# Performance work log

Hardware: AMD Instinct MI355X
Metric: run time of the kernel (lower is better)

## Reference

```python
import jax, jax.numpy as jnp
import numpy as np
import math

B, C, RES, N, H = 32, 32, 16, 16384, 64
G = RES ** 3
RATIO = 1.0


def _halton2(n):
    # 2-D Halton sequence (radical inverse, bases 2 and 3), shape (2, n)
    def radinv(idx, base):
        inv = np.zeros(n, dtype=np.float64)
        f = 1.0 / base
        i = idx.copy()
        while i.max() > 0:
            inv += f * (i % base)
            i //= base
            f /= base
        return inv
    idx = np.arange(1, n + 1)
    return np.stack([radinv(idx, 2), radinv(idx, 3)], axis=0).astype(np.float32)


def setup_inputs() -> dict:
    key = jax.random.key(0)
    ks = jax.random.split(key, 3)
    rng = np.random.default_rng(0)
    x = jax.random.normal(ks[0], (B, C, RES, RES, RES), dtype=jnp.float32)
    # density-driven counts: per-batch multinomial allocation summing exactly to N
    dens = rng.random((B, G)) ** 2
    probs = dens / dens.sum(axis=1, keepdims=True)
    counts = np.stack([rng.multinomial(N, probs[b]) for b in range(B)]).astype(np.int32)
    # grid offsets: ((meshgrid + 0.5) / res - 0.5).view(3, -1)  (normalize_ratio = 0.5)
    grid = np.stack(np.meshgrid(np.arange(RES), np.arange(RES), np.arange(RES), indexing='ij'), 0).astype(np.float32)
    grid_o = ((grid + 0.5) / RES - 0.5).reshape(3, -1)
    # Halton noise scaled: b_rnd * ratio - ratio/2, broadcast to batch
    b_rnd = _halton2(N) * RATIO - RATIO / 2.0
    b_rnd = np.broadcast_to(b_rnd[None], (B, 2, N)).copy()
    # pointwise generator MLP: (C+2) -> H -> 3
    W1 = jax.random.normal(ks[1], (H, C + 2), dtype=jnp.float32) * 0.05
    b1 = jnp.zeros((H,), dtype=jnp.float32)
    W2 = jax.random.normal(ks[2], (3, H), dtype=jnp.float32) * 0.05
    b2 = jnp.zeros((3,), dtype=jnp.float32)
    return {"x": x, "counts": jnp.asarray(counts), "b_rnd": jnp.asarray(b_rnd),
            "grid_o": jnp.asarray(grid_o), "W1": W1, "b1": b1, "W2": W2, "b2": b2}


def reference(x, counts, b_rnd, grid_o, W1, b1, W2, b2):
    b, c = x.shape[0], x.shape[1]
    n = b_rnd.shape[-1]
    xf = x.reshape(b, c, -1)                      # (b, c, G)
    # repeat_interleave(x[:, ind], counts[ind]) with fixed output size n:
    # output slot j maps to cell idx = searchsorted(cumsum(counts), j, 'right')
    cum = jnp.cumsum(counts, axis=1)              # (b, G)
    slots = jnp.arange(n)
    idx = jax.vmap(lambda cs: jnp.searchsorted(cs, slots, side='right'))(cum)  # (b, n)
    x_ind = jnp.take_along_axis(xf, idx[:, None, :], axis=2)                   # (b, c, n)
    o_ind = jnp.transpose(grid_o[:, idx], (1, 0, 2))                           # (b, 3, n)
    b_inp = jnp.concatenate([x_ind, b_rnd], axis=1)                            # (b, c+2, n)
    h = jax.nn.relu(jnp.einsum('hc,bcn->bhn', W1, b_inp) + b1[None, :, None])
    out = jnp.einsum('oh,bhn->bon', W2, h) + b2[None, :, None]                 # (b, 3, n)
    norm = jnp.linalg.norm(out, axis=1)                                        # (b, n)
    reg = jnp.clip(norm - math.sqrt(3.0) / RES, 0.0)
    return out + o_ind, reg
```

## Files before the change

kernel.cpp:

```cpp
#include <hip/hip_runtime.h>
#include <math.h>

constexpr int B_ = 32;
constexpr int C_ = 32;
constexpr int RES_ = 16;
constexpr int G_ = RES_ * RES_ * RES_;
constexpr int N_ = 16384;
constexpr int H_ = 64;
__device__ constexpr float REG_THR = 0.10825317547305483f;

__device__ __forceinline__ unsigned short f2bf(float f) {
    union { float f; unsigned int u; } v; v.f = f;
    const unsigned int r = v.u + 0x7FFFu + ((v.u >> 16) & 1u);
    return (unsigned short)(r >> 16);
}

__global__ __launch_bounds__(256) void scan_kernel(const int* __restrict__ counts,
                                                   int* __restrict__ cum) {
    const int b = blockIdx.x;
    const int* cb = counts + b * G_;
    int* ob = cum + b * G_;

    __shared__ int partials[256];
    const int t = threadIdx.x;
    const int base = t * 16;

    int local[16];
    int s = 0;
#pragma unroll
    for (int i = 0; i < 16; ++i) {
        s += cb[base + i];
        local[i] = s;
    }
    partials[t] = s;
    __syncthreads();

    for (int off = 1; off < 256; off <<= 1) {
        int v = (t >= off) ? partials[t - off] : 0;
        __syncthreads();
        partials[t] += v;
        __syncthreads();
    }
    const int prev = (t > 0) ? partials[t - 1] : 0;

#pragma unroll
    for (int i = 0; i < 16; ++i) ob[base + i] = prev + local[i];
}

constexpr int TCELL = 64;
constexpr int PAD = H_ + 1;
constexpr int WROW = 36;

__global__ __launch_bounds__(256) void hx_kernel(const float* __restrict__ x,
                                                 const float* __restrict__ W1,
                                                 const float* __restrict__ b1,
                                                 unsigned short* __restrict__ hxb) {
    const int b = blockIdx.y;
    const int tile = blockIdx.x * TCELL;
    const int t = threadIdx.x;
    const int cell_l = t & 63;
    const int hh = __builtin_amdgcn_readfirstlane((t >> 6) * 16);

    __shared__ float __align__(16) s_w1[H_ * WROW];
    __shared__ float s_hx[TCELL * PAD];

    for (int i = t; i < H_ * 34; i += 256) {
        const int r = i / 34;
        const int c = i - r * 34;
        s_w1[r * WROW + c] = W1[i];
    }
    if (t < H_) s_w1[t * WROW + 34] = b1[t];

    const float* xb = x + ((size_t)b * C_) * G_ + tile + cell_l;
    float xv[C_];
#pragma unroll
    for (int c = 0; c < C_; ++c) xv[c] = xb[(size_t)c * G_];
    __syncthreads();

    float* row = s_hx + cell_l * PAD + hh;
#pragma unroll 4
    for (int j = 0; j < 16; ++j) {
        const float* w = s_w1 + (hh + j) * WROW;
        float acc = w[34];
#pragma unroll
        for (int c = 0; c < C_; ++c) acc = fmaf(w[c], xv[c], acc);
        row[j] = acc;
    }
    __syncthreads();

    unsigned short* ob = hxb + ((size_t)b * G_ + tile) * H_;
#pragma unroll
    for (int k = 0; k < 2; ++k) {
        const int L = (t + k * 256) * 8;
        const int cell = L >> 6;
        const int h = L & 63;
        const float* s = s_hx + cell * PAD + h;
        unsigned int us[4];
#pragma unroll
        for (int q = 0; q < 4; ++q) {
            const unsigned int lo = f2bf(s[2 * q]);
            const unsigned int hi = f2bf(s[2 * q + 1]);
            us[q] = lo | (hi << 16);
        }
        *(uint4*)(ob + L) = make_uint4(us[0], us[1], us[2], us[3]);
    }
}

__global__ __launch_bounds__(256) void point_kernel(
    const unsigned short* __restrict__ hxb, const float* __restrict__ b_rnd,
    const float* __restrict__ W1, const float* __restrict__ W2,
    const float* __restrict__ b2, const int* __restrict__ cum,
    float* __restrict__ out0, float* __restrict__ reg_out) {
    const int b = blockIdx.y;
    const int n = blockIdx.x * 256 + threadIdx.x;
    const int t = threadIdx.x;

    __shared__ int s_cum[G_];
    const int* cb = cum + b * G_;
#pragma unroll
    for (int i = 0; i < G_ / 256; ++i) s_cum[t + i * 256] = cb[t + i * 256];
    __syncthreads();

    int lo = 0, hi = G_ - 1;
#pragma unroll
    for (int it = 0; it < 12; ++it) {
        const int mid = (lo + hi) >> 1;
        if (s_cum[mid] > n) hi = mid; else lo = mid + 1;
        if (lo >= hi) hi = lo;
    }
    const int idx = lo;

    const float r0 = b_rnd[((size_t)b * 2 + 0) * N_ + n];
    const float r1 = b_rnd[((size_t)b * 2 + 1) * N_ + n];
    const unsigned short* hp = hxb + ((size_t)b * G_ + idx) * H_;

    float o0 = b2[0], o1 = b2[1], o2 = b2[2];
#pragma unroll
    for (int g = 0; g < 8; ++g) {
        const uint4 u = *(const uint4*)(hp + g * 8);
        const unsigned int uw[4] = {u.x, u.y, u.z, u.w};
        float hvv[8];
#pragma unroll
        for (int q = 0; q < 4; ++q) {
            union { unsigned int u; float f; } a, bwd;
            a.u = uw[q] << 16;
            bwd.u = uw[q] & 0xFFFF0000u;
            hvv[2 * q] = a.f;
            hvv[2 * q + 1] = bwd.f;
        }
#pragma unroll
        for (int j = 0; j < 8; ++j) {
            const int h = g * 8 + j;
            float hv = hvv[j];
            hv = fmaf(W1[h * 34 + 32], r0, hv);
            hv = fmaf(W1[h * 34 + 33], r1, hv);
            hv = fmaxf(hv, 0.0f);
            o0 = fmaf(W2[0 * H_ + h], hv, o0);
            o1 = fmaf(W2[1 * H_ + h], hv, o1);
            o2 = fmaf(W2[2 * H_ + h], hv, o2);
        }
    }

    const float nrm = sqrtf(o0 * o0 + o1 * o1 + o2 * o2);
    const float reg = fmaxf(nrm - REG_THR, 0.0f);

    o0 += (float)((idx >> 8) & 15) * 0.0625f - 0.46875f;
    o1 += (float)((idx >> 4) & 15) * 0.0625f - 0.46875f;
    o2 += (float)(idx & 15) * 0.0625f - 0.46875f;

    float* p = out0 + ((size_t)b * 3) * N_ + n;
    p[0]              = o0;
    p[N_]             = o1;
    p[2 * (size_t)N_] = o2;
    reg_out[(size_t)b * N_ + n] = reg;
}

extern "C" void kernel_launch(void* const* d_in, const int* in_sizes, int n_in,
                              void* d_out, int out_size, void* d_ws, size_t ws_size,
                              hipStream_t stream) {
    const float* x      = (const float*)d_in[0];
    const int*   counts = (const int*)  d_in[1];
    const float* b_rnd  = (const float*)d_in[2];
    const float* W1     = (const float*)d_in[4];
    const float* b1     = (const float*)d_in[5];
    const float* W2     = (const float*)d_in[6];
    const float* b2     = (const float*)d_in[7];

    float* out  = (float*)d_out;
    float* rout = out + (size_t)B_ * 3 * N_;

    int* cum = (int*)d_ws;
    unsigned short* hxb =
        (unsigned short*)((char*)d_ws + (size_t)B_ * G_ * sizeof(int));

    scan_kernel<<<B_, 256, 0, stream>>>(counts, cum);

    dim3 gridA(G_ / TCELL, B_);
    hx_kernel<<<gridA, 256, 0, stream>>>(x, W1, b1, hxb);

    dim3 gridB(N_ / 256, B_);
    point_kernel<<<gridB, 256, 0, stream>>>(hxb, b_rnd, W1, W2, b2,
                                            cum, out, rout);
}
```

Measured before the change: 109.5 us.

## Fuse scan into hx kernel, materialize slot-to-cell index, double cells per thread

Drops the separate scan kernel. One extra block per batch in the hx kernel now computes the cumulative counts and writes an explicit per-slot cell index array by expanding the counts. The point kernel reads that index directly, so it no longer stages 4096 cumsum values into shared memory or runs a 12-step binary search. The hx tile is doubled to 128 cells, so each thread computes two cells and reuses its W1 reads from shared memory. The risks are that the serial per-thread fill in the scan block is load-imbalanced, and that more registers per thread may reduce occupancy.

```diff
diff --git a/kernel.cpp b/kernel.cpp
--- a/kernel.cpp
+++ b/kernel.cpp
@@ -15,54 +15,53 @@
     return (unsigned short)(r >> 16);
 }
 
-__global__ __launch_bounds__(256) void scan_kernel(const int* __restrict__ counts,
-                                                   int* __restrict__ cum) {
-    const int b = blockIdx.x;
-    const int* cb = counts + b * G_;
-    int* ob = cum + b * G_;
-
-    __shared__ int partials[256];
-    const int t = threadIdx.x;
-    const int base = t * 16;
-
-    int local[16];
-    int s = 0;
-#pragma unroll
-    for (int i = 0; i < 16; ++i) {
-        s += cb[base + i];
-        local[i] = s;
-    }
-    partials[t] = s;
-    __syncthreads();
-
-    for (int off = 1; off < 256; off <<= 1) {
-        int v = (t >= off) ? partials[t - off] : 0;
-        __syncthreads();
-        partials[t] += v;
-        __syncthreads();
-    }
-    const int prev = (t > 0) ? partials[t - 1] : 0;
-
-#pragma unroll
-    for (int i = 0; i < 16; ++i) ob[base + i] = prev + local[i];
-}
-
-constexpr int TCELL = 64;
+constexpr int TCELL = 128;
 constexpr int PAD = H_ + 1;
 constexpr int WROW = 36;
 
-__global__ __launch_bounds__(256) void hx_kernel(const float* __restrict__ x,
-                                                 const float* __restrict__ W1,
-                                                 const float* __restrict__ b1,
-                                                 unsigned short* __restrict__ hxb) {
+__global__ __launch_bounds__(256) void hx_scan_kernel(
+    const float* __restrict__ x, const float* __restrict__ W1,
+    const float* __restrict__ b1, const int* __restrict__ counts,
+    unsigned short* __restrict__ hxb, int* __restrict__ idxarr) {
     const int b = blockIdx.y;
-    const int tile = blockIdx.x * TCELL;
     const int t = threadIdx.x;
-    const int cell_l = t & 63;
-    const int hh = __builtin_amdgcn_readfirstlane((t >> 6) * 16);
 
     __shared__ float __align__(16) s_w1[H_ * WROW];
     __shared__ float s_hx[TCELL * PAD];
+
+    if (blockIdx.x == G_ / TCELL) {
+        int* partials = (int*)s_w1;
+        const int* cb = counts + b * G_;
+        const int base = t * 16;
+        int local[16];
+        int s = 0;
+#pragma unroll
+        for (int i = 0; i < 16; ++i) { s += cb[base + i]; local[i] = s; }
+        partials[t] = s;
+        __syncthreads();
+        for (int off = 1; off < 256; off <<= 1) {
+            int v = (t >= off) ? partials[t - off] : 0;
+            __syncthreads();
+            partials[t] += v;
+            __syncthreads();
+        }
+        const int prev = (t > 0) ? partials[t - 1] : 0;
+
+        int* ib = idxarr + b * N_;
+        int startk = prev;
+#pragma unroll
+        for (int i = 0; i < 16; ++i) {
+            const int endk = prev + local[i];
+            const int cell = base + i;
+            for (int k = startk; k < endk; ++k) ib[k] = cell;
+            startk = endk;
+        }
+        return;
+    }
+
+    const int tile = blockIdx.x * TCELL;
+    const int cell_l = t & 63;
+    const int hh = __builtin_amdgcn_readfirstlane((t >> 6) * 16);
 
     for (int i = t; i < H_ * 34; i += 256) {
         const int r = i / 34;
@@ -72,25 +71,34 @@
     if (t < H_) s_w1[t * WROW + 34] = b1[t];
 
     const float* xb = x + ((size_t)b * C_) * G_ + tile + cell_l;
-    float xv[C_];
+    float xv0[C_], xv1[C_];
 #pragma unroll
-    for (int c = 0; c < C_; ++c) xv[c] = xb[(size_t)c * G_];
+    for (int c = 0; c < C_; ++c) {
+        xv0[c] = xb[(size_t)c * G_];
+        xv1[c] = xb[(size_t)c * G_ + 64];
+    }
     __syncthreads();
 
-    float* row = s_hx + cell_l * PAD + hh;
+    float* row0 = s_hx + cell_l * PAD + hh;
+    float* row1 = s_hx + (cell_l + 64) * PAD + hh;
 #pragma unroll 4
     for (int j = 0; j < 16; ++j) {
         const float* w = s_w1 + (hh + j) * WROW;
-        float acc = w[34];
+        float a0 = w[34];
+        float a1 = a0;
 #pragma unroll
-        for (int c = 0; c < C_; ++c) acc = fmaf(w[c], xv[c], acc);
-        row[j] = acc;
+        for (int c = 0; c < C_; ++c) {
+            a0 = fmaf(w[c], xv0[c], a0);
+            a1 = fmaf(w[c], xv1[c], a1);
+        }
+        row0[j] = a0;
+        row1[j] = a1;
     }
     __syncthreads();
 
     unsigned short* ob = hxb + ((size_t)b * G_ + tile) * H_;
 #pragma unroll
-    for (int k = 0; k < 2; ++k) {
+    for (int k = 0; k < 4; ++k) {
         const int L = (t + k * 256) * 8;
         const int cell = L >> 6;
         const int h = L & 63;
@@ -109,27 +117,12 @@
 __global__ __launch_bounds__(256) void point_kernel(
     const unsigned short* __restrict__ hxb, const float* __restrict__ b_rnd,
     const float* __restrict__ W1, const float* __restrict__ W2,
-    const float* __restrict__ b2, const int* __restrict__ cum,
+    const float* __restrict__ b2, const int* __restrict__ idxarr,
     float* __restrict__ out0, float* __restrict__ reg_out) {
     const int b = blockIdx.y;
     const int n = blockIdx.x * 256 + threadIdx.x;
-    const int t = threadIdx.x;
 
-    __shared__ int s_cum[G_];
-    const int* cb = cum + b * G_;
-#pragma unroll
-    for (int i = 0; i < G_ / 256; ++i) s_cum[t + i * 256] = cb[t + i * 256];
-    __syncthreads();
-
-    int lo = 0, hi = G_ - 1;
-#pragma unroll
-    for (int it = 0; it < 12; ++it) {
-        const int mid = (lo + hi) >> 1;
-        if (s_cum[mid] > n) hi = mid; else lo = mid + 1;
-        if (lo >= hi) hi = lo;
-    }
-    const int idx = lo;
-
+    const int idx = idxarr[(size_t)b * N_ + n];
     const float r0 = b_rnd[((size_t)b * 2 + 0) * N_ + n];
     const float r1 = b_rnd[((size_t)b * 2 + 1) * N_ + n];
     const unsigned short* hp = hxb + ((size_t)b * G_ + idx) * H_;
@@ -189,16 +182,14 @@
     float* out  = (float*)d_out;
     float* rout = out + (size_t)B_ * 3 * N_;
 
-    int* cum = (int*)d_ws;
+    int* idxarr = (int*)d_ws;
     unsigned short* hxb =
-        (unsigned short*)((char*)d_ws + (size_t)B_ * G_ * sizeof(int));
+        (unsigned short*)((char*)d_ws + (size_t)B_ * N_ * sizeof(int));
 
-    scan_kernel<<<B_, 256, 0, stream>>>(counts, cum);
-
-    dim3 gridA(G_ / TCELL, B_);
-    hx_kernel<<<gridA, 256, 0, stream>>>(x, W1, b1, hxb);
+    dim3 gridA(G_ / TCELL + 1, B_);
+    hx_scan_kernel<<<gridA, 256, 0, stream>>>(x, W1, b1, counts, hxb, idxarr);
 
     dim3 gridB(N_ / 256, B_);
     point_kernel<<<gridB, 256, 0, stream>>>(hxb, b_rnd, W1, W2, b2,
-                                            cum, out, rout);
+                                            idxarr, out, rout);
 }
```

After: 109.9 us. About the same (+0.3%).
